# Optimization experiments

Measured on AMD Instinct MI355X. Metric: run time of the kernel, lower is better.

## Reference

```python
import jax, jax.numpy as jnp
import numpy as np

B, T, C = 64, 512, 384
H = 6
HD = C // H  # 64
FF = 4 * C
EPS = 1e-5


def _rope(x):
    # x: [B,H,T,D]. Faithful to source: fres = 1/1000^(arange(0,D,2)//D) == all ones
    # (integer floor division), so the rotation angle is just the position t.
    t = jnp.arange(x.shape[2], dtype=jnp.float32)
    cos = jnp.cos(t)[None, None, :, None]
    sin = jnp.sin(t)[None, None, :, None]
    xr = x[..., 0::2]
    xi = x[..., 1::2]
    outr = cos * xr - sin * xi
    outi = sin * xr + cos * xi
    return jnp.stack([outr, outi], axis=-1).reshape(x.shape)


def _mha(x, qw, qb, kw, kb, vw, vb, pw, pb):
    # per-head projections batched over H: [B,T,C] x [H,C,D] -> [B,H,T,D]
    q = jnp.einsum('btc,hcd->bhtd', x, qw) + qb[None, :, None, :]
    k = jnp.einsum('btc,hcd->bhtd', x, kw) + kb[None, :, None, :]
    v = jnp.einsum('btc,hcd->bhtd', x, vw) + vb[None, :, None, :]
    q = _rope(q)
    k = _rope(k)
    # NOTE: source scales by C**-0.5 with C = n_embed (384), not head_size.
    wei = jnp.einsum('bhtd,bhsd->bhts', q, k) * (C ** -0.5)
    Tq = x.shape[1]
    causal = jnp.tril(jnp.ones((Tq, Tq), dtype=bool))
    wei = jnp.where(causal[None, None], wei, -jnp.inf)
    wei = jax.nn.softmax(wei, axis=-1)
    out = jnp.einsum('bhts,bhsd->bhtd', wei, v)
    out = out.transpose(0, 2, 1, 3).reshape(x.shape[0], Tq, C)  # concat heads
    return out @ pw + pb


def _ln(x, g, b):
    m = jnp.mean(x, axis=-1, keepdims=True)
    var = jnp.mean((x - m) ** 2, axis=-1, keepdims=True)
    return g * (x - m) / jnp.sqrt(var + EPS) + b


def setup_inputs() -> dict:
    key = jax.random.key(0)
    ks = jax.random.split(key, 16)
    s = 0.02
    d = {
        'x': jax.random.normal(ks[0], (B, T, C), dtype=jnp.float32),
        'q1_w': jax.random.normal(ks[1], (H, C, HD)) * s, 'q1_b': jnp.zeros((H, HD)),
        'k1_w': jax.random.normal(ks[2], (H, C, HD)) * s, 'k1_b': jnp.zeros((H, HD)),
        'v1_w': jax.random.normal(ks[3], (H, C, HD)) * s, 'v1_b': jnp.zeros((H, HD)),
        'p1_w': jax.random.normal(ks[4], (C, C)) * s, 'p1_b': jnp.zeros((C,)),
        'ln1_g': jnp.ones((C,)), 'ln1_b': jnp.zeros((C,)),
        'q2_w': jax.random.normal(ks[5], (H, C, HD)) * s, 'q2_b': jnp.zeros((H, HD)),
        'k2_w': jax.random.normal(ks[6], (H, C, HD)) * s, 'k2_b': jnp.zeros((H, HD)),
        'v2_w': jax.random.normal(ks[7], (H, C, HD)) * s, 'v2_b': jnp.zeros((H, HD)),
        'p2_w': jax.random.normal(ks[8], (C, C)) * s, 'p2_b': jnp.zeros((C,)),
        'ln2_g': jnp.ones((C,)), 'ln2_b': jnp.zeros((C,)),
        'f1_w': jax.random.normal(ks[9], (C, FF)) * s, 'f1_b': jnp.zeros((FF,)),
        'f2_w': jax.random.normal(ks[10], (FF, C)) * s, 'f2_b': jnp.zeros((C,)),
        'ln3_g': jnp.ones((C,)), 'ln3_b': jnp.zeros((C,)),
    }
    return {k2: jnp.asarray(v, jnp.float32) for k2, v in d.items()}


def reference(x, q1_w, q1_b, k1_w, k1_b, v1_w, v1_b, p1_w, p1_b, ln1_g, ln1_b,
              q2_w, q2_b, k2_w, k2_b, v2_w, v2_b, p2_w, p2_b, ln2_g, ln2_b,
              f1_w, f1_b, f2_w, f2_b, ln3_g, ln3_b):
    attn1 = _mha(x, q1_w, q1_b, k1_w, k1_b, v1_w, v1_b, p1_w, p1_b)
    out1 = _ln(x + attn1, ln1_g, ln1_b)
    attn2 = _mha(out1, q2_w, q2_b, k2_w, k2_b, v2_w, v2_b, p2_w, p2_b)
    out2 = _ln(out1 + attn2, ln2_g, ln2_b)
    ff = jax.nn.relu(out2 @ f1_w + f1_b) @ f2_w + f2_b
    return _ln(out2 + ff, ln3_g, ln3_b)
```

## Files before the change

### kernel.cpp

```cpp
#include <hip/hip_runtime.h>
#include <cstddef>
#include <cstdint>

#define B_ 64
#define T_ 512
#define C_ 384
#define H_ 6
#define HD_ 64
#define FF_ 1536

typedef unsigned short u16;
typedef __attribute__((ext_vector_type(8))) __bf16 bf16x8;
typedef __attribute__((ext_vector_type(8))) short short8;
typedef __attribute__((ext_vector_type(4))) float f32x4;

#define MFMA_BF16(a, b, c) __builtin_amdgcn_mfma_f32_16x16x32_bf16((a), (b), (c), 0, 0, 0)

__device__ __forceinline__ u16 f2bf(float f) {
    union { float f; unsigned u; } x; x.f = f;
    unsigned r = x.u + 0x7fff + ((x.u >> 16) & 1);
    return (u16)(r >> 16);
}

__device__ __forceinline__ void gload16(const u16* g, u16* l) {
    __builtin_amdgcn_global_load_lds(
        (const __attribute__((address_space(1))) void*)g,
        (__attribute__((address_space(3))) void*)l, 16, 0, 0);
}

__global__ __launch_bounds__(256)
void prep_kernel(const float* __restrict__ q1w, const float* __restrict__ k1w, const float* __restrict__ v1w,
                 const float* __restrict__ q2w, const float* __restrict__ k2w, const float* __restrict__ v2w,
                 const float* __restrict__ p1w, const float* __restrict__ p2w,
                 const float* __restrict__ f1w, const float* __restrict__ f2w,
                 const float* __restrict__ q1b, const float* __restrict__ k1b, const float* __restrict__ v1b,
                 const float* __restrict__ q2b, const float* __restrict__ k2b, const float* __restrict__ v2b,
                 u16* wq1, u16* wq2, u16* p1t, u16* p2t, u16* f1t, u16* f2t,
                 float* bq1, float* bq2, float* cst, float* snt)
{
    const int job = blockIdx.y;
    const int idx = blockIdx.x * 256 + threadIdx.x;
    if (job <= 1) {
        if (idx >= 1152 * 384) return;
        const int n = idx / 384, k = idx - n * 384;
        const int which = n / 384 + 0;
        const int w2 = n >> 7;
        (void)which; (void)w2;
        const int wsel = n / 384;
        const int rest = n - wsel * 384;
        const int h = rest >> 6, d = rest & 63;
        const float* src;
        if (job == 0) src = (wsel == 0 ? q1w : wsel == 1 ? k1w : v1w);
        else          src = (wsel == 0 ? q2w : wsel == 1 ? k2w : v2w);
        const float v = src[((size_t)h * 384 + k) * 64 + d];
        (job == 0 ? wq1 : wq2)[idx] = f2bf(v);
    } else if (job <= 3) {
        if (idx >= 384 * 384) return;
        const int n = idx / 384, k = idx - n * 384;
        const float* src = (job == 2 ? p1w : p2w);
        (job == 2 ? p1t : p2t)[idx] = f2bf(src[(size_t)k * 384 + n]);
    } else if (job == 4) {
        if (idx >= 1536 * 384) return;
        const int n = idx / 384, k = idx - n * 384;
        f1t[idx] = f2bf(f1w[(size_t)k * 1536 + n]);
    } else if (job == 5) {
        if (idx >= 384 * 1536) return;
        const int n = idx / 1536, k = idx - n * 1536;
        f2t[idx] = f2bf(f2w[(size_t)k * 384 + n]);
    } else {
        if (idx < 1152) {
            const int wsel = idx / 384, r = idx - wsel * 384;
            bq1[idx] = (wsel == 0 ? q1b : wsel == 1 ? k1b : v1b)[r];
        } else if (idx < 2304) {
            const int j = idx - 1152;
            const int wsel = j / 384, r = j - wsel * 384;
            bq2[j] = (wsel == 0 ? q2b : wsel == 1 ? k2b : v2b)[r];
        } else if (idx < 2816) {
            const int t = idx - 2304; cst[t] = cosf((float)t);
        } else if (idx < 3328) {
            const int t = idx - 2816; snt[t] = sinf((float)t);
        }
    }
}

__global__ __launch_bounds__(256)
void cast_kernel(const float* __restrict__ in, u16* __restrict__ out, int n4)
{
    int i = blockIdx.x * 256 + threadIdx.x;
    const int stride = gridDim.x * 256;
    for (; i < n4; i += stride) {
        float4 v = *reinterpret_cast<const float4*>(&in[(size_t)i * 4]);
        ushort4 o;
        o.x = f2bf(v.x); o.y = f2bf(v.y); o.z = f2bf(v.z); o.w = f2bf(v.w);
        *reinterpret_cast<ushort4*>(&out[(size_t)i * 4]) = o;
    }
}

template<int EPI>
__global__ __launch_bounds__(256)
void gemm_mfma(const u16* __restrict__ A, const u16* __restrict__ Bt, int K,
               const float* __restrict__ bias, const float* __restrict__ res,
               float* __restrict__ outf, u16* __restrict__ outb,
               u16* __restrict__ qo, u16* __restrict__ ko, u16* __restrict__ vo,
               const float* __restrict__ cst, const float* __restrict__ snt,
               int N)
{
    __shared__ u16 As[128 * 32];
    __shared__ u16 Bs[128 * 32];
    const int tid = threadIdx.x;
    const int w = tid >> 6, lane = tid & 63;
    const int m0 = blockIdx.x * 128, n0 = blockIdx.y * 128;
    const int wm = w >> 1, wn = w & 1;
    const int c = lane & 15, g = lane >> 4;

    const u16* gA = A + (size_t)(m0 + w * 16 + (lane >> 2)) * K + (lane & 3) * 8;
    const u16* gB = Bt + (size_t)(n0 + w * 16 + (lane >> 2)) * K + (lane & 3) * 8;
    u16* lA = As + w * 512;
    u16* lB = Bs + w * 512;

    f32x4 acc[4][4];
    #pragma unroll
    for (int i = 0; i < 4; ++i)
        #pragma unroll
        for (int j = 0; j < 4; ++j) acc[i][j] = (f32x4)0.0f;

    for (int k0 = 0; k0 < K; k0 += 32) {
        __syncthreads();
        gload16(gA + k0, lA);
        gload16(gA + k0 + (size_t)64 * K, lA + 64 * 32);
        gload16(gB + k0, lB);
        gload16(gB + k0 + (size_t)64 * K, lB + 64 * 32);
        __syncthreads();
        bf16x8 af[4], bf[4];
        #pragma unroll
        for (int fi = 0; fi < 4; ++fi)
            af[fi] = *(const bf16x8*)&As[(wm * 64 + fi * 16 + c) * 32 + g * 8];
        #pragma unroll
        for (int fj = 0; fj < 4; ++fj)
            bf[fj] = *(const bf16x8*)&Bs[(wn * 64 + fj * 16 + c) * 32 + g * 8];
        #pragma unroll
        for (int fi = 0; fi < 4; ++fi)
            #pragma unroll
            for (int fj = 0; fj < 4; ++fj)
                acc[fi][fj] = MFMA_BF16(af[fi], bf[fj], acc[fi][fj]);
    }

    if (EPI == 0) {
        const int which = blockIdx.y / 3;
        u16* dst = (which == 0 ? qo : which == 1 ? ko : vo);
        #pragma unroll
        for (int fi = 0; fi < 4; ++fi) {
            #pragma unroll
            for (int r = 0; r < 4; ++r) {
                const int m = m0 + wm * 64 + fi * 16 + 4 * g + r;
                const int t = m & 511, bb = m >> 9;
                const float cs = cst[t], sn = snt[t];
                #pragma unroll
                for (int fj = 0; fj < 4; ++fj) {
                    const int n = n0 + wn * 64 + fj * 16 + c;
                    float v = acc[fi][fj][r] + bias[n];
                    const float vp = __shfl_xor(v, 1);
                    float ov;
                    if (which < 2)
                        ov = ((n & 1) == 0) ? cs * v - sn * vp : sn * vp + cs * v;
                    else
                        ov = v;
                    const int rest = n - which * 384;
                    const int h = rest >> 6, d = rest & 63;
                    dst[(((size_t)bb * H_ + h) * T_ + t) * 64 + d] = f2bf(ov);
                }
            }
        }
    } else {
        #pragma unroll
        for (int fi = 0; fi < 4; ++fi) {
            #pragma unroll
            for (int r = 0; r < 4; ++r) {
                const int m = m0 + wm * 64 + fi * 16 + 4 * g + r;
                #pragma unroll
                for (int fj = 0; fj < 4; ++fj) {
                    const int n = n0 + wn * 64 + fj * 16 + c;
                    float v = acc[fi][fj][r] + bias[n];
                    if (EPI == 1) {
                        v += res[(size_t)m * N + n];
                        outf[(size_t)m * N + n] = v;
                    } else {
                        outb[(size_t)m * N + n] = f2bf(fmaxf(v, 0.0f));
                    }
                }
            }
        }
    }
}

#define KS_B(r, chB) ((r) * 176 + (chB) * 16)
#define VT_B(d, t)   ((d) * 176 + ((((t) >> 3) ^ ((d) & 7) ^ ((d) >> 3)) << 4) + (((t) & 7) << 1))

__global__ __launch_bounds__(256)
void attn_mfma(const u16* __restrict__ Q, const u16* __restrict__ K,
               const u16* __restrict__ V, u16* __restrict__ out)
{
    __shared__ u16 Ks[64 * 88];
    __shared__ u16 Vt[64 * 88];
    __shared__ u16 Ps[4][16 * 88];

    const int qt = blockIdx.x, h = blockIdx.y, b = blockIdx.z;
    const int tid = threadIdx.x;
    const int w = tid >> 6, lane = tid & 63;
    const int c = lane & 15, g = lane >> 4;
    const size_t base = ((size_t)b * H_ + h) * T_ * 64;
    const int qrow0 = qt * 64 + w * 16;
    const float scale = 0.05103103630798288f;

    bf16x8 qf[2];
    #pragma unroll
    for (int kh = 0; kh < 2; ++kh)
        qf[kh] = *(const bf16x8*)&Q[base + (size_t)(qrow0 + c) * 64 + kh * 32 + g * 8];

    f32x4 O[4];
    float m_[4], l_[4];
    #pragma unroll
    for (int i = 0; i < 4; ++i) { O[i] = (f32x4)0.0f; m_[i] = -INFINITY; l_[i] = 0.0f; }

    u16* Pw = Ps[w];

    for (int kt = 0; kt <= qt; ++kt) {
        __syncthreads();
        #pragma unroll
        for (int s = 0; s < 2; ++s) {
            const int idx = tid + s * 256;
            const int r = idx >> 3, ch = idx & 7;
            const size_t gsrc = base + (size_t)(kt * 64 + r) * 64 + ch * 8;
            short8 kv = *(const short8*)&K[gsrc];
            *(short8*)((char*)Ks + KS_B(r, ch)) = kv;
            short8 vv = *(const short8*)&V[gsrc];
            #pragma unroll
            for (int j = 0; j < 8; ++j)
                *(u16*)((char*)Vt + VT_B(ch * 8 + j, r)) = (u16)vv[j];
        }
        __syncthreads();

        f32x4 S[4];
        #pragma unroll
        for (int fc = 0; fc < 4; ++fc) {
            S[fc] = (f32x4)0.0f;
            #pragma unroll
            for (int kh = 0; kh < 2; ++kh) {
                bf16x8 kf = *(const bf16x8*)((char*)Ks + KS_B(fc * 16 + c, kh * 4 + g));
                S[fc] = MFMA_BF16(qf[kh], kf, S[fc]);
            }
        }

        const bool diag = (kt == qt);
        #pragma unroll
        for (int r = 0; r < 4; ++r) {
            const int qloc = w * 16 + 4 * g + r;
            float mx = -INFINITY;
            #pragma unroll
            for (int fc = 0; fc < 4; ++fc) {
                float sv = S[fc][r] * scale;
                if (diag && (fc * 16 + c > qloc)) sv = -INFINITY;
                S[fc][r] = sv;
                mx = fmaxf(mx, sv);
            }
            #pragma unroll
            for (int off = 1; off < 16; off <<= 1)
                mx = fmaxf(mx, __shfl_xor(mx, off, 16));
            const float mnew = fmaxf(m_[r], mx);
            const float corr = __expf(m_[r] - mnew);
            m_[r] = mnew;
            float su = 0.0f;
            #pragma unroll
            for (int fc = 0; fc < 4; ++fc) {
                const float p = __expf(S[fc][r] - mnew);
                S[fc][r] = p; su += p;
            }
            #pragma unroll
            for (int off = 1; off < 16; off <<= 1)
                su += __shfl_xor(su, off, 16);
            l_[r] = l_[r] * corr + su;
            #pragma unroll
            for (int fd = 0; fd < 4; ++fd) O[fd][r] *= corr;
        }

        #pragma unroll
        for (int fc = 0; fc < 4; ++fc)
            #pragma unroll
            for (int r = 0; r < 4; ++r)
                *(u16*)((char*)Pw + (4 * g + r) * 176 + (fc * 16 + c) * 2) = f2bf(S[fc][r]);

        bf16x8 pa[2];
        #pragma unroll
        for (int kh = 0; kh < 2; ++kh)
            pa[kh] = *(const bf16x8*)((char*)Pw + c * 176 + kh * 64 + g * 16);
        #pragma unroll
        for (int fd = 0; fd < 4; ++fd) {
            const int d = fd * 16 + c;
            #pragma unroll
            for (int kh = 0; kh < 2; ++kh) {
                const int kb = kh * 4 + g;
                bf16x8 vf = *(const bf16x8*)((char*)Vt + d * 176 + (((kb) ^ (d & 7) ^ (d >> 3)) << 4));
                O[fd] = MFMA_BF16(pa[kh], vf, O[fd]);
            }
        }
    }

    #pragma unroll
    for (int r = 0; r < 4; ++r) {
        const int t = qrow0 + 4 * g + r;
        const float inv = 1.0f / l_[r];
        const size_t o = ((size_t)b * T_ + t) * C_ + h * 64;
        #pragma unroll
        for (int fd = 0; fd < 4; ++fd)
            out[o + fd * 16 + c] = f2bf(O[fd][r] * inv);
    }
}

__global__ __launch_bounds__(256)
void ln_kernel(const float* __restrict__ in, const float* __restrict__ gam,
               const float* __restrict__ bta, float* __restrict__ outf,
               u16* __restrict__ outb)
{
    const int lane = threadIdx.x & 63;
    const int wv   = threadIdx.x >> 6;
    const size_t row = (size_t)blockIdx.x * 4 + wv;
    const float* x = in + row * C_;

    float vals[6];
    float s = 0.0f;
    #pragma unroll
    for (int i = 0; i < 6; ++i) { vals[i] = x[lane + i * 64]; s += vals[i]; }
    #pragma unroll
    for (int off = 1; off < 64; off <<= 1) s += __shfl_xor(s, off, 64);
    const float mean = s * (1.0f / 384.0f);

    float vs = 0.0f;
    #pragma unroll
    for (int i = 0; i < 6; ++i) { const float d = vals[i] - mean; vs += d * d; }
    #pragma unroll
    for (int off = 1; off < 64; off <<= 1) vs += __shfl_xor(vs, off, 64);
    const float inv = rsqrtf(vs * (1.0f / 384.0f) + 1e-5f);

    #pragma unroll
    for (int i = 0; i < 6; ++i) {
        const int cc = lane + i * 64;
        const float y = gam[cc] * (vals[i] - mean) * inv + bta[cc];
        if (outf) outf[row * C_ + cc] = y;
        if (outb) outb[row * C_ + cc] = f2bf(y);
    }
}

extern "C" void kernel_launch(void* const* d_in, const int* in_sizes, int n_in,
                              void* d_out, int out_size, void* d_ws, size_t ws_size,
                              hipStream_t stream)
{
    const float* x    = (const float*)d_in[0];
    const float* q1w  = (const float*)d_in[1];  const float* q1b = (const float*)d_in[2];
    const float* k1w  = (const float*)d_in[3];  const float* k1b = (const float*)d_in[4];
    const float* v1w  = (const float*)d_in[5];  const float* v1b = (const float*)d_in[6];
    const float* p1w  = (const float*)d_in[7];  const float* p1b = (const float*)d_in[8];
    const float* ln1g = (const float*)d_in[9];  const float* ln1b = (const float*)d_in[10];
    const float* q2w  = (const float*)d_in[11]; const float* q2b = (const float*)d_in[12];
    const float* k2w  = (const float*)d_in[13]; const float* k2b = (const float*)d_in[14];
    const float* v2w  = (const float*)d_in[15]; const float* v2b = (const float*)d_in[16];
    const float* p2w  = (const float*)d_in[17]; const float* p2b = (const float*)d_in[18];
    const float* ln2g = (const float*)d_in[19]; const float* ln2b = (const float*)d_in[20];
    const float* f1w  = (const float*)d_in[21]; const float* f1b = (const float*)d_in[22];
    const float* f2w  = (const float*)d_in[23]; const float* f2b = (const float*)d_in[24];
    const float* ln3g = (const float*)d_in[25]; const float* ln3b = (const float*)d_in[26];

    const size_t WQKV = 1152 * 384, WP = 384 * 384, WF = 1536 * 384;
    u16* wq1 = (u16*)d_ws;
    u16* wq2 = wq1 + WQKV;
    u16* p1t = wq2 + WQKV;
    u16* p2t = p1t + WP;
    u16* f1t = p2t + WP;
    u16* f2t = f1t + WF;
    float* bq1 = (float*)(f2t + WF);
    float* bq2 = bq1 + 1152;
    float* cst = bq2 + 1152;
    float* snt = cst + 512;
    u16* chunkBase = (u16*)(snt + 512);
    const size_t fixedBytes = (size_t)((char*)chunkBase - (char*)d_ws);

    int CB = 64;
    while (CB > 1 && fixedBytes + 20ull * CB * T_ * C_ > ws_size) CB >>= 1;
    const size_t McC = (size_t)CB * T_ * C_;
    const int Mc = CB * T_;

    u16* sQ  = chunkBase;
    u16* sK  = sQ + McC;
    u16* sV  = sK + McC;
    u16* sAb = sV + McC;
    u16* sX  = sAb + McC;
    u16* sO2 = sX + McC;
    u16* tmp = sQ;
    float* bufF  = (float*)(sO2 + McC);
    float* out1f = bufF + McC;

    const dim3 blk(256);

    prep_kernel<<<dim3(2304, 7), blk, 0, stream>>>(
        q1w, k1w, v1w, q2w, k2w, v2w, p1w, p2w, f1w, f2w,
        q1b, k1b, v1b, q2b, k2b, v2b,
        wq1, wq2, p1t, p2t, f1t, f2t, bq1, bq2, cst, snt);

    for (int b0 = 0; b0 < B_; b0 += CB) {
        const float* xc = x + (size_t)b0 * T_ * C_;
        float*       oc = (float*)d_out + (size_t)b0 * T_ * C_;

        cast_kernel<<<dim3(2048), blk, 0, stream>>>(xc, sX, (int)(McC / 4));

        gemm_mfma<0><<<dim3(Mc / 128, 9), blk, 0, stream>>>(sX, wq1, 384, bq1,
            nullptr, nullptr, nullptr, sQ, sK, sV, cst, snt, 1152);
        attn_mfma<<<dim3(T_ / 64, H_, CB), blk, 0, stream>>>(sQ, sK, sV, sAb);
        gemm_mfma<1><<<dim3(Mc / 128, 3), blk, 0, stream>>>(sAb, p1t, 384, p1b,
            xc, bufF, nullptr, nullptr, nullptr, nullptr, cst, snt, 384);
        ln_kernel<<<dim3(Mc / 4), blk, 0, stream>>>(bufF, ln1g, ln1b, out1f, sX);

        gemm_mfma<0><<<dim3(Mc / 128, 9), blk, 0, stream>>>(sX, wq2, 384, bq2,
            nullptr, nullptr, nullptr, sQ, sK, sV, cst, snt, 1152);
        attn_mfma<<<dim3(T_ / 64, H_, CB), blk, 0, stream>>>(sQ, sK, sV, sAb);
        gemm_mfma<1><<<dim3(Mc / 128, 3), blk, 0, stream>>>(sAb, p2t, 384, p2b,
            out1f, bufF, nullptr, nullptr, nullptr, nullptr, cst, snt, 384);
        ln_kernel<<<dim3(Mc / 4), blk, 0, stream>>>(bufF, ln2g, ln2b, oc, sO2);

        gemm_mfma<2><<<dim3(Mc / 128, 12), blk, 0, stream>>>(sO2, f1t, 384, f1b,
            nullptr, nullptr, tmp, nullptr, nullptr, nullptr, cst, snt, 1536);
        gemm_mfma<1><<<dim3(Mc / 128, 3), blk, 0, stream>>>(tmp, f2t, 1536, f2b,
            oc, bufF, nullptr, nullptr, nullptr, nullptr, cst, snt, 384);
        ln_kernel<<<dim3(Mc / 4), blk, 0, stream>>>(bufF, ln3g, ln3b, oc, nullptr);
    }
}
```

Before: 852.8 us.

## Fuse projection GEMMs with residual and LayerNorm, swizzle LDS, pack bf16 stores

Adds a gemm_ln kernel in which each 128-thread block computes a full 64x384 output row tile, so the bias, residual add and LayerNorm run in the epilogue. This removes the separate ln_kernel launches and the fp32 round trip through an intermediate buffer. It also applies an XOR swizzle to the LDS tiles in gemm_mfma to reduce bank conflicts, and packs pairs of bf16 outputs into 32-bit stores. The trade-off is that the fused kernel holds 48 accumulator vectors per thread, which raises register pressure, and it launches fewer, larger blocks.

```diff
diff --git a/kernel.cpp b/kernel.cpp
--- a/kernel.cpp
+++ b/kernel.cpp
@@ -10,6 +10,7 @@
 #define FF_ 1536
 
 typedef unsigned short u16;
+typedef unsigned int u32;
 typedef __attribute__((ext_vector_type(8))) __bf16 bf16x8;
 typedef __attribute__((ext_vector_type(8))) short short8;
 typedef __attribute__((ext_vector_type(4))) float f32x4;
@@ -27,6 +28,8 @@
         (const __attribute__((address_space(1))) void*)g,
         (__attribute__((address_space(3))) void*)l, 16, 0, 0);
 }
+
+__device__ __forceinline__ int swz4(int row, int ch) { return ch ^ ((row >> 1) & 3); }
 
 __global__ __launch_bounds__(256)
 void prep_kernel(const float* __restrict__ q1w, const float* __restrict__ k1w, const float* __restrict__ v1w,
@@ -43,17 +46,13 @@
     if (job <= 1) {
         if (idx >= 1152 * 384) return;
         const int n = idx / 384, k = idx - n * 384;
-        const int which = n / 384 + 0;
-        const int w2 = n >> 7;
-        (void)which; (void)w2;
         const int wsel = n / 384;
         const int rest = n - wsel * 384;
         const int h = rest >> 6, d = rest & 63;
         const float* src;
         if (job == 0) src = (wsel == 0 ? q1w : wsel == 1 ? k1w : v1w);
         else          src = (wsel == 0 ? q2w : wsel == 1 ? k2w : v2w);
-        const float v = src[((size_t)h * 384 + k) * 64 + d];
-        (job == 0 ? wq1 : wq2)[idx] = f2bf(v);
+        (job == 0 ? wq1 : wq2)[idx] = f2bf(src[((size_t)h * 384 + k) * 64 + d]);
     } else if (job <= 3) {
         if (idx >= 384 * 384) return;
         const int n = idx / 384, k = idx - n * 384;
@@ -99,8 +98,8 @@
 template<int EPI>
 __global__ __launch_bounds__(256)
 void gemm_mfma(const u16* __restrict__ A, const u16* __restrict__ Bt, int K,
-               const float* __restrict__ bias, const float* __restrict__ res,
-               float* __restrict__ outf, u16* __restrict__ outb,
+               const float* __restrict__ bias,
+               u16* __restrict__ outb,
                u16* __restrict__ qo, u16* __restrict__ ko, u16* __restrict__ vo,
                const float* __restrict__ cst, const float* __restrict__ snt,
                int N)
@@ -112,9 +111,11 @@
     const int m0 = blockIdx.x * 128, n0 = blockIdx.y * 128;
     const int wm = w >> 1, wn = w & 1;
     const int c = lane & 15, g = lane >> 4;
-
-    const u16* gA = A + (size_t)(m0 + w * 16 + (lane >> 2)) * K + (lane & 3) * 8;
-    const u16* gB = Bt + (size_t)(n0 + w * 16 + (lane >> 2)) * K + (lane & 3) * 8;
+    const int cs = (c >> 1) & 3;
+
+    const int srow = w * 16 + (lane >> 2);
+    const u16* gA = A + (size_t)(m0 + srow) * K + swz4(srow, lane & 3) * 8;
+    const u16* gB = Bt + (size_t)(n0 + srow) * K + swz4(srow, lane & 3) * 8;
     u16* lA = As + w * 512;
     u16* lB = Bs + w * 512;
 
@@ -131,18 +132,18 @@
         gload16(gB + k0, lB);
         gload16(gB + k0 + (size_t)64 * K, lB + 64 * 32);
         __syncthreads();
-        bf16x8 af[4], bf[4];
+        bf16x8 af[4], bfr[4];
         #pragma unroll
         for (int fi = 0; fi < 4; ++fi)
-            af[fi] = *(const bf16x8*)&As[(wm * 64 + fi * 16 + c) * 32 + g * 8];
+            af[fi] = *(const bf16x8*)&As[(wm * 64 + fi * 16 + c) * 32 + (g ^ cs) * 8];
         #pragma unroll
         for (int fj = 0; fj < 4; ++fj)
-            bf[fj] = *(const bf16x8*)&Bs[(wn * 64 + fj * 16 + c) * 32 + g * 8];
+            bfr[fj] = *(const bf16x8*)&Bs[(wn * 64 + fj * 16 + c) * 32 + (g ^ cs) * 8];
         #pragma unroll
         for (int fi = 0; fi < 4; ++fi)
             #pragma unroll
             for (int fj = 0; fj < 4; ++fj)
-                acc[fi][fj] = MFMA_BF16(af[fi], bf[fj], acc[fi][fj]);
+                acc[fi][fj] = MFMA_BF16(af[fi], bfr[fj], acc[fi][fj]);
     }
 
     if (EPI == 0) {
@@ -154,7 +155,7 @@
             for (int r = 0; r < 4; ++r) {
                 const int m = m0 + wm * 64 + fi * 16 + 4 * g + r;
                 const int t = m & 511, bb = m >> 9;
-                const float cs = cst[t], sn = snt[t];
+                const float csn = cst[t], sn = snt[t];
                 #pragma unroll
                 for (int fj = 0; fj < 4; ++fj) {
                     const int n = n0 + wn * 64 + fj * 16 + c;
@@ -162,12 +163,16 @@
                     const float vp = __shfl_xor(v, 1);
                     float ov;
                     if (which < 2)
-                        ov = ((n & 1) == 0) ? cs * v - sn * vp : sn * vp + cs * v;
+                        ov = ((n & 1) == 0) ? csn * v - sn * vp : sn * vp + csn * v;
                     else
                         ov = v;
-                    const int rest = n - which * 384;
-                    const int h = rest >> 6, d = rest & 63;
-                    dst[(((size_t)bb * H_ + h) * T_ + t) * 64 + d] = f2bf(ov);
+                    const float op = __shfl_xor(ov, 1);
+                    if ((c & 1) == 0) {
+                        const int rest = n - which * 384;
+                        const int h = rest >> 6, d = rest & 63;
+                        const u32 pk = (u32)f2bf(ov) | ((u32)f2bf(op) << 16);
+                        *(u32*)&dst[(((size_t)bb * H_ + h) * T_ + t) * 64 + d] = pk;
+                    }
                 }
             }
         }
@@ -180,14 +185,92 @@
                 #pragma unroll
                 for (int fj = 0; fj < 4; ++fj) {
                     const int n = n0 + wn * 64 + fj * 16 + c;
-                    float v = acc[fi][fj][r] + bias[n];
-                    if (EPI == 1) {
-                        v += res[(size_t)m * N + n];
-                        outf[(size_t)m * N + n] = v;
-                    } else {
-                        outb[(size_t)m * N + n] = f2bf(fmaxf(v, 0.0f));
+                    float v = fmaxf(acc[fi][fj][r] + bias[n], 0.0f);
+                    const float vn = __shfl_xor(v, 1);
+                    if ((c & 1) == 0) {
+                        const u32 pk = (u32)f2bf(v) | ((u32)f2bf(vn) << 16);
+                        *(u32*)&outb[(size_t)m * N + n] = pk;
                     }
                 }
+            }
+        }
+    }
+}
+
+template<int KK>
+__global__ __launch_bounds__(128, 2)
+void gemm_ln(const u16* __restrict__ A, const u16* __restrict__ Bt,
+             const float* __restrict__ bias, const float* __restrict__ res,
+             const float* __restrict__ lng, const float* __restrict__ lnb,
+             float* __restrict__ yf, u16* __restrict__ yb)
+{
+    __shared__ u16 As[64 * 32];
+    __shared__ u16 Bs[384 * 32];
+    const int tid = threadIdx.x;
+    const int w = tid >> 6, lane = tid & 63;
+    const int c = lane & 15, g = lane >> 4;
+    const int cs = (c >> 1) & 3;
+    const int m0 = blockIdx.x * 64;
+    const int sr = tid >> 2, sch = tid & 3;
+
+    f32x4 acc0[24], acc1[24];
+    #pragma unroll
+    for (int fn = 0; fn < 24; ++fn) { acc0[fn] = (f32x4)0.0f; acc1[fn] = (f32x4)0.0f; }
+
+    #pragma unroll 2
+    for (int k0 = 0; k0 < KK; k0 += 32) {
+        __syncthreads();
+        #pragma unroll
+        for (int i = 0; i < 2; ++i) {
+            const int row = sr + i * 32;
+            gload16(A + (size_t)(m0 + row) * KK + k0 + swz4(row, sch) * 8,
+                    As + (size_t)(i * 128 + w * 64) * 8);
+        }
+        #pragma unroll
+        for (int i = 0; i < 12; ++i) {
+            const int row = sr + i * 32;
+            gload16(Bt + (size_t)row * KK + k0 + swz4(row, sch) * 8,
+                    Bs + (size_t)(i * 128 + w * 64) * 8);
+        }
+        __syncthreads();
+        const bf16x8 a0 = *(const bf16x8*)&As[(w * 32 + c) * 32 + (g ^ cs) * 8];
+        const bf16x8 a1 = *(const bf16x8*)&As[(w * 32 + 16 + c) * 32 + (g ^ cs) * 8];
+        #pragma unroll
+        for (int fn = 0; fn < 24; ++fn) {
+            const bf16x8 bfr = *(const bf16x8*)&Bs[(fn * 16 + c) * 32 + (g ^ cs) * 8];
+            acc0[fn] = MFMA_BF16(a0, bfr, acc0[fn]);
+            acc1[fn] = MFMA_BF16(a1, bfr, acc1[fn]);
+        }
+    }
+
+    #pragma unroll
+    for (int mi = 0; mi < 2; ++mi) {
+        #pragma unroll
+        for (int r = 0; r < 4; ++r) {
+            const int row = m0 + w * 32 + mi * 16 + 4 * g + r;
+            float vals[24];
+            float s = 0.0f, s2 = 0.0f;
+            #pragma unroll
+            for (int fn = 0; fn < 24; ++fn) {
+                const int col = fn * 16 + c;
+                float v = (mi ? acc1[fn][r] : acc0[fn][r]) + bias[col]
+                          + res[(size_t)row * 384 + col];
+                vals[fn] = v; s += v; s2 += v * v;
+            }
+            #pragma unroll
+            for (int off = 1; off < 16; off <<= 1) {
+                s  += __shfl_xor(s, off);
+                s2 += __shfl_xor(s2, off);
+            }
+            const float mean = s * (1.0f / 384.0f);
+            const float var  = s2 * (1.0f / 384.0f) - mean * mean;
+            const float inv  = rsqrtf(var + 1e-5f);
+            #pragma unroll
+            for (int fn = 0; fn < 24; ++fn) {
+                const int col = fn * 16 + c;
+                const float y = lng[col] * (vals[fn] - mean) * inv + lnb[col];
+                yf[(size_t)row * 384 + col] = y;
+                if (yb) yb[(size_t)row * 384 + col] = f2bf(y);
             }
         }
     }
@@ -313,40 +396,6 @@
         #pragma unroll
         for (int fd = 0; fd < 4; ++fd)
             out[o + fd * 16 + c] = f2bf(O[fd][r] * inv);
-    }
-}
-
-__global__ __launch_bounds__(256)
-void ln_kernel(const float* __restrict__ in, const float* __restrict__ gam,
-               const float* __restrict__ bta, float* __restrict__ outf,
-               u16* __restrict__ outb)
-{
-    const int lane = threadIdx.x & 63;
-    const int wv   = threadIdx.x >> 6;
-    const size_t row = (size_t)blockIdx.x * 4 + wv;
-    const float* x = in + row * C_;
-
-    float vals[6];
-    float s = 0.0f;
-    #pragma unroll
-    for (int i = 0; i < 6; ++i) { vals[i] = x[lane + i * 64]; s += vals[i]; }
-    #pragma unroll
-    for (int off = 1; off < 64; off <<= 1) s += __shfl_xor(s, off, 64);
-    const float mean = s * (1.0f / 384.0f);
-
-    float vs = 0.0f;
-    #pragma unroll
-    for (int i = 0; i < 6; ++i) { const float d = vals[i] - mean; vs += d * d; }
-    #pragma unroll
-    for (int off = 1; off < 64; off <<= 1) vs += __shfl_xor(vs, off, 64);
-    const float inv = rsqrtf(vs * (1.0f / 384.0f) + 1e-5f);
-
-    #pragma unroll
-    for (int i = 0; i < 6; ++i) {
-        const int cc = lane + i * 64;
-        const float y = gam[cc] * (vals[i] - mean) * inv + bta[cc];
-        if (outf) outf[row * C_ + cc] = y;
-        if (outb) outb[row * C_ + cc] = f2bf(y);
     }
 }
 
@@ -395,8 +444,8 @@
     u16* sX  = sAb + McC;
     u16* sO2 = sX + McC;
     u16* tmp = sQ;
-    float* bufF  = (float*)(sO2 + McC);
-    float* out1f = bufF + McC;
+    float* y1f = (float*)(sO2 + McC);
+    float* y2f = y1f + McC;
 
     const dim3 blk(256);
 
@@ -412,23 +461,20 @@
         cast_kernel<<<dim3(2048), blk, 0, stream>>>(xc, sX, (int)(McC / 4));
 
         gemm_mfma<0><<<dim3(Mc / 128, 9), blk, 0, stream>>>(sX, wq1, 384, bq1,
-            nullptr, nullptr, nullptr, sQ, sK, sV, cst, snt, 1152);
+            nullptr, sQ, sK, sV, cst, snt, 1152);
         attn_mfma<<<dim3(T_ / 64, H_, CB), blk, 0, stream>>>(sQ, sK, sV, sAb);
-        gemm_mfma<1><<<dim3(Mc / 128, 3), blk, 0, stream>>>(sAb, p1t, 384, p1b,
-            xc, bufF, nullptr, nullptr, nullptr, nullptr, cst, snt, 384);
-        ln_kernel<<<dim3(Mc / 4), blk, 0, stream>>>(bufF, ln1g, ln1b, out1f, sX);
+        gemm_ln<384><<<dim3(Mc / 64), dim3(128), 0, stream>>>(sAb, p1t, p1b, xc,
+            ln1g, ln1b, y1f, sX);
 
         gemm_mfma<0><<<dim3(Mc / 128, 9), blk, 0, stream>>>(sX, wq2, 384, bq2,
-            nullptr, nullptr, nullptr, sQ, sK, sV, cst, snt, 1152);
+            nullptr, sQ, sK, sV, cst, snt, 1152);
         attn_mfma<<<dim3(T_ / 64, H_, CB), blk, 0, stream>>>(sQ, sK, sV, sAb);
-        gemm_mfma<1><<<dim3(Mc / 128, 3), blk, 0, stream>>>(sAb, p2t, 384, p2b,
-            out1f, bufF, nullptr, nullptr, nullptr, nullptr, cst, snt, 384);
-        ln_kernel<<<dim3(Mc / 4), blk, 0, stream>>>(bufF, ln2g, ln2b, oc, sO2);
+        gemm_ln<384><<<dim3(Mc / 64), dim3(128), 0, stream>>>(sAb, p2t, p2b, y1f,
+            ln2g, ln2b, y2f, sO2);
 
         gemm_mfma<2><<<dim3(Mc / 128, 12), blk, 0, stream>>>(sO2, f1t, 384, f1b,
-            nullptr, nullptr, tmp, nullptr, nullptr, nullptr, cst, snt, 1536);
-        gemm_mfma<1><<<dim3(Mc / 128, 3), blk, 0, stream>>>(tmp, f2t, 1536, f2b,
-            oc, bufF, nullptr, nullptr, nullptr, nullptr, cst, snt, 384);
-        ln_kernel<<<dim3(Mc / 4), blk, 0, stream>>>(bufF, ln3g, ln3b, oc, nullptr);
-    }
-}
+            tmp, nullptr, nullptr, nullptr, cst, snt, 1536);
+        gemm_ln<1536><<<dim3(Mc / 64), dim3(128), 0, stream>>>(tmp, f2t, f2b, y2f,
+            ln3g, ln3b, oc, nullptr);
+    }
+}
```

Measured after the change: 873.9 us. 2.5% more time.

## Double-buffer GEMM LDS tiles with XOR swizzle and packed bf16 epilogue stores

Applied to the files above, without the earlier changes.

The MFMA GEMM now double-buffers its A/B shared-memory tiles, so the global-to-LDS load of the next K-slice is issued before the MFMAs on the current one, and only one barrier per iteration remains. LDS chunks are XOR-swizzled by row to cut bank conflicts on the bf16x8 fragment reads. The QKV/RoPE and ReLU epilogues exchange neighbour values by shuffle and write two bf16 values as one 32-bit store. The cost is twice the LDS per block and possible occupancy loss, plus extra shuffles in the epilogue.

```diff
diff --git a/kernel.cpp b/kernel.cpp
--- a/kernel.cpp
+++ b/kernel.cpp
@@ -10,6 +10,7 @@
 #define FF_ 1536
 
 typedef unsigned short u16;
+typedef unsigned int u32;
 typedef __attribute__((ext_vector_type(8))) __bf16 bf16x8;
 typedef __attribute__((ext_vector_type(8))) short short8;
 typedef __attribute__((ext_vector_type(4))) float f32x4;
@@ -27,6 +28,8 @@
         (const __attribute__((address_space(1))) void*)g,
         (__attribute__((address_space(3))) void*)l, 16, 0, 0);
 }
+
+__device__ __forceinline__ int swz4(int row, int ch) { return ch ^ ((row >> 1) & 3); }
 
 __global__ __launch_bounds__(256)
 void prep_kernel(const float* __restrict__ q1w, const float* __restrict__ k1w, const float* __restrict__ v1w,
@@ -43,17 +46,13 @@
     if (job <= 1) {
         if (idx >= 1152 * 384) return;
         const int n = idx / 384, k = idx - n * 384;
-        const int which = n / 384 + 0;
-        const int w2 = n >> 7;
-        (void)which; (void)w2;
         const int wsel = n / 384;
         const int rest = n - wsel * 384;
         const int h = rest >> 6, d = rest & 63;
         const float* src;
         if (job == 0) src = (wsel == 0 ? q1w : wsel == 1 ? k1w : v1w);
         else          src = (wsel == 0 ? q2w : wsel == 1 ? k2w : v2w);
-        const float v = src[((size_t)h * 384 + k) * 64 + d];
-        (job == 0 ? wq1 : wq2)[idx] = f2bf(v);
+        (job == 0 ? wq1 : wq2)[idx] = f2bf(src[((size_t)h * 384 + k) * 64 + d]);
     } else if (job <= 3) {
         if (idx >= 384 * 384) return;
         const int n = idx / 384, k = idx - n * 384;
@@ -105,18 +104,19 @@
                const float* __restrict__ cst, const float* __restrict__ snt,
                int N)
 {
-    __shared__ u16 As[128 * 32];
-    __shared__ u16 Bs[128 * 32];
+    __shared__ u16 As[2][128 * 32];
+    __shared__ u16 Bs[2][128 * 32];
     const int tid = threadIdx.x;
     const int w = tid >> 6, lane = tid & 63;
     const int m0 = blockIdx.x * 128, n0 = blockIdx.y * 128;
     const int wm = w >> 1, wn = w & 1;
     const int c = lane & 15, g = lane >> 4;
-
-    const u16* gA = A + (size_t)(m0 + w * 16 + (lane >> 2)) * K + (lane & 3) * 8;
-    const u16* gB = Bt + (size_t)(n0 + w * 16 + (lane >> 2)) * K + (lane & 3) * 8;
-    u16* lA = As + w * 512;
-    u16* lB = Bs + w * 512;
+    const int cs = (c >> 1) & 3;
+
+    const int srow = w * 16 + (lane >> 2);
+    const u16* gA = A + (size_t)(m0 + srow) * K + swz4(srow, lane & 3) * 8;
+    const u16* gB = Bt + (size_t)(n0 + srow) * K + swz4(srow, lane & 3) * 8;
+    const int ldst = w * 512;
 
     f32x4 acc[4][4];
     #pragma unroll
@@ -124,25 +124,36 @@
         #pragma unroll
         for (int j = 0; j < 4; ++j) acc[i][j] = (f32x4)0.0f;
 
-    for (int k0 = 0; k0 < K; k0 += 32) {
+    const int NT = K >> 5;
+
+    gload16(gA, As[0] + ldst);
+    gload16(gA + (size_t)64 * K, As[0] + 64 * 32 + ldst);
+    gload16(gB, Bs[0] + ldst);
+    gload16(gB + (size_t)64 * K, Bs[0] + 64 * 32 + ldst);
+    __syncthreads();
+
+    for (int t = 0; t < NT; ++t) {
+        const int cur = t & 1;
+        if (t + 1 < NT) {
+            const int k0 = (t + 1) * 32;
+            gload16(gA + k0, As[cur ^ 1] + ldst);
+            gload16(gA + k0 + (size_t)64 * K, As[cur ^ 1] + 64 * 32 + ldst);
+            gload16(gB + k0, Bs[cur ^ 1] + ldst);
+            gload16(gB + k0 + (size_t)64 * K, Bs[cur ^ 1] + 64 * 32 + ldst);
+        }
+        bf16x8 af[4], bfr[4];
+        #pragma unroll
+        for (int fi = 0; fi < 4; ++fi)
+            af[fi] = *(const bf16x8*)&As[cur][(wm * 64 + fi * 16 + c) * 32 + (g ^ cs) * 8];
+        #pragma unroll
+        for (int fj = 0; fj < 4; ++fj)
+            bfr[fj] = *(const bf16x8*)&Bs[cur][(wn * 64 + fj * 16 + c) * 32 + (g ^ cs) * 8];
+        #pragma unroll
+        for (int fi = 0; fi < 4; ++fi)
+            #pragma unroll
+            for (int fj = 0; fj < 4; ++fj)
+                acc[fi][fj] = MFMA_BF16(af[fi], bfr[fj], acc[fi][fj]);
         __syncthreads();
-        gload16(gA + k0, lA);
-        gload16(gA + k0 + (size_t)64 * K, lA + 64 * 32);
-        gload16(gB + k0, lB);
-        gload16(gB + k0 + (size_t)64 * K, lB + 64 * 32);
-        __syncthreads();
-        bf16x8 af[4], bf[4];
-        #pragma unroll
-        for (int fi = 0; fi < 4; ++fi)
-            af[fi] = *(const bf16x8*)&As[(wm * 64 + fi * 16 + c) * 32 + g * 8];
-        #pragma unroll
-        for (int fj = 0; fj < 4; ++fj)
-            bf[fj] = *(const bf16x8*)&Bs[(wn * 64 + fj * 16 + c) * 32 + g * 8];
-        #pragma unroll
-        for (int fi = 0; fi < 4; ++fi)
-            #pragma unroll
-            for (int fj = 0; fj < 4; ++fj)
-                acc[fi][fj] = MFMA_BF16(af[fi], bf[fj], acc[fi][fj]);
     }
 
     if (EPI == 0) {
@@ -154,7 +165,7 @@
             for (int r = 0; r < 4; ++r) {
                 const int m = m0 + wm * 64 + fi * 16 + 4 * g + r;
                 const int t = m & 511, bb = m >> 9;
-                const float cs = cst[t], sn = snt[t];
+                const float csn = cst[t], sn = snt[t];
                 #pragma unroll
                 for (int fj = 0; fj < 4; ++fj) {
                     const int n = n0 + wn * 64 + fj * 16 + c;
@@ -162,16 +173,20 @@
                     const float vp = __shfl_xor(v, 1);
                     float ov;
                     if (which < 2)
-                        ov = ((n & 1) == 0) ? cs * v - sn * vp : sn * vp + cs * v;
+                        ov = ((n & 1) == 0) ? csn * v - sn * vp : sn * vp + csn * v;
                     else
                         ov = v;
-                    const int rest = n - which * 384;
-                    const int h = rest >> 6, d = rest & 63;
-                    dst[(((size_t)bb * H_ + h) * T_ + t) * 64 + d] = f2bf(ov);
+                    const float op = __shfl_xor(ov, 1);
+                    if ((c & 1) == 0) {
+                        const int rest = n - which * 384;
+                        const int h = rest >> 6, d = rest & 63;
+                        const u32 pk = (u32)f2bf(ov) | ((u32)f2bf(op) << 16);
+                        *(u32*)&dst[(((size_t)bb * H_ + h) * T_ + t) * 64 + d] = pk;
+                    }
                 }
             }
         }
-    } else {
+    } else if (EPI == 1) {
         #pragma unroll
         for (int fi = 0; fi < 4; ++fi) {
             #pragma unroll
@@ -180,12 +195,25 @@
                 #pragma unroll
                 for (int fj = 0; fj < 4; ++fj) {
                     const int n = n0 + wn * 64 + fj * 16 + c;
-                    float v = acc[fi][fj][r] + bias[n];
-                    if (EPI == 1) {
-                        v += res[(size_t)m * N + n];
-                        outf[(size_t)m * N + n] = v;
-                    } else {
-                        outb[(size_t)m * N + n] = f2bf(fmaxf(v, 0.0f));
+                    float v = acc[fi][fj][r] + bias[n] + res[(size_t)m * N + n];
+                    outf[(size_t)m * N + n] = v;
+                }
+            }
+        }
+    } else {
+        #pragma unroll
+        for (int fi = 0; fi < 4; ++fi) {
+            #pragma unroll
+            for (int r = 0; r < 4; ++r) {
+                const int m = m0 + wm * 64 + fi * 16 + 4 * g + r;
+                #pragma unroll
+                for (int fj = 0; fj < 4; ++fj) {
+                    const int n = n0 + wn * 64 + fj * 16 + c;
+                    float v = fmaxf(acc[fi][fj][r] + bias[n], 0.0f);
+                    const float vn = __shfl_xor(v, 1);
+                    if ((c & 1) == 0) {
+                        const u32 pk = (u32)f2bf(v) | ((u32)f2bf(vn) << 16);
+                        *(u32*)&outb[(size_t)m * N + n] = pk;
                     }
                 }
             }
@@ -395,8 +423,8 @@
     u16* sX  = sAb + McC;
     u16* sO2 = sX + McC;
     u16* tmp = sQ;
-    float* bufF  = (float*)(sO2 + McC);
-    float* out1f = bufF + McC;
+    float* bufF = (float*)(sO2 + McC);
+    float* y1f  = bufF + McC;
 
     const dim3 blk(256);
 
@@ -416,13 +444,13 @@
         attn_mfma<<<dim3(T_ / 64, H_, CB), blk, 0, stream>>>(sQ, sK, sV, sAb);
         gemm_mfma<1><<<dim3(Mc / 128, 3), blk, 0, stream>>>(sAb, p1t, 384, p1b,
             xc, bufF, nullptr, nullptr, nullptr, nullptr, cst, snt, 384);
-        ln_kernel<<<dim3(Mc / 4), blk, 0, stream>>>(bufF, ln1g, ln1b, out1f, sX);
+        ln_kernel<<<dim3(Mc / 4), blk, 0, stream>>>(bufF, ln1g, ln1b, y1f, sX);
 
         gemm_mfma<0><<<dim3(Mc / 128, 9), blk, 0, stream>>>(sX, wq2, 384, bq2,
             nullptr, nullptr, nullptr, sQ, sK, sV, cst, snt, 1152);
         attn_mfma<<<dim3(T_ / 64, H_, CB), blk, 0, stream>>>(sQ, sK, sV, sAb);
         gemm_mfma<1><<<dim3(Mc / 128, 3), blk, 0, stream>>>(sAb, p2t, 384, p2b,
-            out1f, bufF, nullptr, nullptr, nullptr, nullptr, cst, snt, 384);
+            y1f, bufF, nullptr, nullptr, nullptr, nullptr, cst, snt, 384);
         ln_kernel<<<dim3(Mc / 4), blk, 0, stream>>>(bufF, ln2g, ln2b, oc, sO2);
 
         gemm_mfma<2><<<dim3(Mc / 128, 12), blk, 0, stream>>>(sO2, f1t, 384, f1b,
```

Measured after the change: 814.6 us. 4.5% less time.
